# Performance work log

Measured on AMD Instinct MI355X. Metric: run time of the kernel, lower is better.

The kernel has to match this reference:

```python
import jax, jax.numpy as jnp
import numpy as np

N, C, L, E = 10000, 128, 9, 5  # nodes, channels, (lmax+1)^2, num_elements
INV_SQRT_C = 1.0 / np.sqrt(C).astype(np.float32)


def _sparse(key, shape, p=0.15):
    # mimic the sparsity of e3nn CG coupling (U) tensors
    k1, k2 = jax.random.split(key)
    mask = jax.random.bernoulli(k1, p, shape)
    vals = jax.random.normal(k2, shape, dtype=jnp.float32)
    return jnp.where(mask, vals, 0.0)


def setup_inputs() -> dict:
    key = jax.random.key(0)
    ks = jax.random.split(key, 16)
    node_feats = jax.random.normal(ks[0], (N, C, L), dtype=jnp.float32)
    node_attrs = jax.nn.one_hot(jax.random.randint(ks[1], (N,), 0, E), E, dtype=jnp.float32)
    sc = jax.random.normal(ks[2], (N, 512), dtype=jnp.float32)
    # CG coupling tensors U_nu per output irrep (constant buffers in the torch module)
    # l_out = 0 (d=1): path counts k3=10, k2=3, k1=1
    U3_0 = _sparse(ks[3], (1, L, L, L, 10))
    U2_0 = _sparse(ks[4], (1, L, L, 3))
    U1_0 = _sparse(ks[5], (1, L, 1))
    # l_out = 1 (d=3): path counts k3=12, k2=4, k1=1
    U3_1 = _sparse(ks[6], (3, L, L, L, 12))
    U2_1 = _sparse(ks[7], (3, L, L, 4))
    U1_1 = _sparse(ks[8], (3, L, 1))
    # element-dependent contraction weights: randn(E, k, C) / k  (MACE init)
    w3_0 = jax.random.normal(ks[9], (E, 10, C), dtype=jnp.float32) / 10.0
    w2_0 = jax.random.normal(ks[10], (E, 3, C), dtype=jnp.float32) / 3.0
    w1_0 = jax.random.normal(ks[11], (E, 1, C), dtype=jnp.float32) / 1.0
    w3_1 = jax.random.normal(ks[12], (E, 12, C), dtype=jnp.float32) / 12.0
    w2_1 = jax.random.normal(ks[13], (E, 4, C), dtype=jnp.float32) / 4.0
    w1_1 = jax.random.normal(ks[14], (E, 1, C), dtype=jnp.float32) / 1.0
    # o3.Linear internal weights (one [C,C] block per output irrep)
    kl0, kl1 = jax.random.split(ks[15])
    lin_w0 = jax.random.normal(kl0, (C, C), dtype=jnp.float32)
    lin_w1 = jax.random.normal(kl1, (C, C), dtype=jnp.float32)
    return dict(node_feats=node_feats, node_attrs=node_attrs, sc=sc,
                U3_0=U3_0, U2_0=U2_0, U1_0=U1_0, w3_0=w3_0, w2_0=w2_0, w1_0=w1_0,
                U3_1=U3_1, U2_1=U2_1, U1_1=U1_1, w3_1=w3_1, w2_1=w2_1, w1_1=w1_1,
                lin_w0=lin_w0, lin_w1=lin_w1)


def _contraction(x, y, U3, U2, U1, w3, w2, w1):
    # MACE recursive symmetric contraction, correlation=3.
    # x: [N,C,L] node feats, y: [N,E] one-hot, U_nu: [d, L^nu, k_nu], w_nu: [E,k_nu,C]
    out = jnp.einsum('duvwk,ekc,bcw,be->bcduv', U3, w3, x, y)      # [N,C,d,L,L]
    c2 = jnp.einsum('duvk,ekc,be->bcduv', U2, w2, y) + out
    out = jnp.einsum('bcduv,bcv->bcdu', c2, x)                      # [N,C,d,L]
    c1 = jnp.einsum('duk,ekc,be->bcdu', U1, w1, y) + out
    out = jnp.einsum('bcdu,bcu->bcd', c1, x)                        # [N,C,d]
    return out.reshape(out.shape[0], -1)                            # [N,C*d]


def reference(node_feats, node_attrs, sc,
              U3_0, U2_0, U1_0, w3_0, w2_0, w1_0,
              U3_1, U2_1, U1_1, w3_1, w2_1, w1_1,
              lin_w0, lin_w1):
    # SymmetricContraction: one Contraction per target irrep, concat over irreps
    out0 = _contraction(node_feats, node_attrs, U3_0, U2_0, U1_0, w3_0, w2_0, w1_0)  # [N,C]
    out1 = _contraction(node_feats, node_attrs, U3_1, U2_1, U1_1, w3_1, w2_1, w1_1)  # [N,3C]
    # o3.Linear(target_irreps, target_irreps): per-l channel mixing, 1/sqrt(fan_in)
    y0 = (out0 @ lin_w0) * INV_SQRT_C                                # [N,C]
    x1 = out1.reshape(-1, C, 3)
    y1 = jnp.einsum('bcd,ce->bed', x1, lin_w1) * INV_SQRT_C          # [N,C,3]
    out = jnp.concatenate([y0, y1.reshape(-1, 3 * C)], axis=-1)      # [N,512]
    return out + sc  # use_sc residual
```

## Files before the change

### kernel.cpp

```cpp
#include <hip/hip_runtime.h>


#define CCH 128
#define LDIM 9
#define NE 5
#define BLK 256
#define NCPT 4
#define TSTR 220
#define TGSTR 880
#define U3LDS 8748

__global__ __launch_bounds__(BLK) void count_offs_kernel(
    const float* __restrict__ attrs, int N,
    int* __restrict__ elem, int* __restrict__ gcnt,
    int* __restrict__ offs, int* __restrict__ cur) {
  int n = blockIdx.x * BLK + threadIdx.x;
  int e = 0;
  if (n < N) {
    const float* a = attrs + n * NE;
#pragma unroll
    for (int j = 1; j < NE; ++j)
      if (a[j] > 0.5f) e = j;
    elem[n] = e;
  }
  int lane = threadIdx.x & 63;
#pragma unroll
  for (int k = 0; k < NE; ++k) {
    unsigned long long m = __ballot(n < N && e == k);
    if (m) {
      int leader = __ffsll((long long)m) - 1;
      if (lane == leader) atomicAdd(&gcnt[k], __popcll(m));
    }
  }
  __threadfence();
  __syncthreads();
  if (threadIdx.x == 0) {
    int t = atomicAdd(&gcnt[NE], 1);
    if (t == (int)gridDim.x - 1) {
      int acc = 0;
      for (int k = 0; k < NE; ++k) {
        int ck = atomicAdd(&gcnt[k], 0);
        offs[k] = acc; cur[k] = acc; acc += ck;
      }
      offs[NE] = acc;
    }
  }
}

__global__ __launch_bounds__(BLK) void scatter_kernel(
    const int* __restrict__ elem, int N,
    int* __restrict__ cur, int* __restrict__ order) {
  int n = blockIdx.x * BLK + threadIdx.x;
  if (n >= N) return;
  int e = elem[n];
  int lane = threadIdx.x & 63;
#pragma unroll
  for (int k = 0; k < NE; ++k) {
    if (e == k) {
      unsigned long long m = __ballot(1);
      int cnt = __popcll(m);
      int leader = __ffsll((long long)m) - 1;
      int base = 0;
      if (lane == leader) base = atomicAdd(&cur[k], cnt);
      base = __shfl(base, leader);
      int rank = __popcll(m & ((1ull << lane) - 1ull));
      order[base + rank] = n;
    }
  }
}

__global__ __launch_bounds__(BLK) void table_kernel(
    const float* __restrict__ U3_0, const float* __restrict__ U2_0,
    const float* __restrict__ U1_0, const float* __restrict__ U3_1,
    const float* __restrict__ U2_1, const float* __restrict__ U1_1,
    const float* __restrict__ w3_0, const float* __restrict__ w2_0,
    const float* __restrict__ w1_0, const float* __restrict__ w3_1,
    const float* __restrict__ w2_1, const float* __restrict__ w1_1,
    float* __restrict__ table) {
  const int b = blockIdx.x;
  const int dd = blockIdx.y;
  const int e = b / CCH, c = b % CCH;
  float* Tg = table + (size_t)b * TGSTR + dd * TSTR;
  __shared__ float Us[U3LDS];
  __shared__ float U2s[324];
  __shared__ float R3[729];
  __shared__ float R2[81];
  __shared__ float R1l[9];
  __shared__ float w3l[12], w2l[4];
  const int tid = threadIdx.x;
  const int d = dd - 1;
  const int K3 = (dd == 0) ? 10 : 12;
  const int K2 = (dd == 0) ? 3 : 4;

  if (dd == 0) {
    for (int i = tid; i < 7290; i += BLK) Us[i] = U3_0[i];
    for (int i = tid; i < 243; i += BLK)  U2s[i] = U2_0[i];
    if (tid < 10) w3l[tid] = w3_0[(e * 10 + tid) * CCH + c];
    else if (tid < 13) w2l[tid - 10] = w2_0[(e * 3 + (tid - 10)) * CCH + c];
    if (tid < 9) R1l[tid] = U1_0[tid] * w1_0[e * CCH + c];
  } else {
    for (int i = tid; i < 8748; i += BLK) Us[i] = U3_1[d * 8748 + i];
    for (int i = tid; i < 324; i += BLK)  U2s[i] = U2_1[d * 324 + i];
    if (tid < 12) w3l[tid] = w3_1[(e * 12 + tid) * CCH + c];
    else if (tid < 16) w2l[tid - 12] = w2_1[(e * 4 + (tid - 12)) * CCH + c];
    if (tid < 9) R1l[tid] = U1_1[d * 9 + tid] * w1_1[e * CCH + c];
  }
  __syncthreads();
  for (int r = tid; r < 729; r += BLK) {
    float acc = 0.f;
    for (int k = 0; k < K3; ++k) acc += Us[r * K3 + k] * w3l[k];
    R3[r] = acc;
  }
  for (int q = tid; q < 81; q += BLK) {
    float acc = 0.f;
    for (int k = 0; k < K2; ++k) acc += U2s[q * K2 + k] * w2l[k];
    R2[q] = acc;
  }
  __syncthreads();
  for (int i = tid; i < TSTR; i += BLK) {
    float val = 0.f;
    if (i < 219) {
      int rem = i, u = 0;
      while (rem >= (10 - u) * (11 - u) / 2) {
        rem -= (10 - u) * (11 - u) / 2; ++u;
      }
      if (rem == 0) {
        val = R1l[u];
      } else {
        rem -= 1;
        int v = u;
        while (rem >= 10 - v) { rem -= 10 - v; ++v; }
        if (rem == 0) {
          val = (u == v) ? R2[u * 9 + v] : R2[u * 9 + v] + R2[v * 9 + u];
        } else {
          int w = v + (rem - 1);
          if (u == v && v == w)
            val = R3[(u * 9 + u) * 9 + u];
          else if (u == v)
            val = R3[(u * 9 + u) * 9 + w] + R3[(u * 9 + w) * 9 + u] +
                  R3[(w * 9 + u) * 9 + u];
          else if (v == w)
            val = R3[(u * 9 + v) * 9 + v] + R3[(v * 9 + u) * 9 + v] +
                  R3[(v * 9 + v) * 9 + u];
          else
            val = R3[(u * 9 + v) * 9 + w] + R3[(u * 9 + w) * 9 + v] +
                  R3[(v * 9 + u) * 9 + w] + R3[(v * 9 + w) * 9 + u] +
                  R3[(w * 9 + u) * 9 + v] + R3[(w * 9 + v) * 9 + u];
        }
      }
    }
    Tg[i] = val;
  }
}

__global__ __launch_bounds__(BLK, 6) void contract_kernel(
    const float* __restrict__ feats, const float* __restrict__ table,
    const int* __restrict__ order, const int* __restrict__ offs,
    float* __restrict__ tmp, int NPAD) {
  const int cg = blockIdx.x, e = blockIdx.z;
  const int c0 = cg * NCPT;
  const int start = offs[e], end = offs[e + 1];
  const int pbase = start + blockIdx.y * BLK;
  if (pbase >= end) return;
  const int p = pbase + threadIdx.x;
  const bool valid = (p < end);
  const int n = order[valid ? p : (end - 1)];

  float tf[NCPT * LDIM];
  {
    const float4* xp =
        (const float4*)(feats + ((size_t)n * CCH + c0) * LDIM);
#pragma unroll
    for (int q = 0; q < 9; ++q) *(float4*)&tf[4 * q] = xp[q];
  }

  const float* Te = table + (size_t)(e * CCH + c0) * TGSTR;

#pragma unroll 1
  for (int dd = 0; dd < 4; ++dd) {
    float accd[NCPT];
#pragma unroll
    for (int c = 0; c < NCPT; ++c) {
      const float* B = Te + (size_t)c * TGSTR + dd * TSTR;
      int idx = 0;
      float acc = 0.f;
#pragma unroll
      for (int u = 0; u < 9; ++u) {
        float inner = B[idx++];
#pragma unroll
        for (int v = u; v < 9; ++v) {
          float Hv = B[idx++];
#pragma unroll
          for (int w = v; w < 9; ++w)
            Hv = fmaf(B[idx++], tf[c * LDIM + w], Hv);
          inner = fmaf(Hv, tf[c * LDIM + v], inner);
        }
        acc = fmaf(inner, tf[c * LDIM + u], acc);
      }
      accd[c] = acc;
    }
    if (valid) {
      float* o = tmp + ((size_t)dd * CCH + c0) * NPAD + p;
#pragma unroll
      for (int c = 0; c < NCPT; ++c) o[(size_t)c * NPAD] = accd[c];
    }
  }
}

#define NB 8
__global__ __launch_bounds__(BLK, 6) void linear_kernel(
    const float* __restrict__ tmp, const float* __restrict__ W0,
    const float* __restrict__ W1, const float* __restrict__ sc,
    const int* __restrict__ order, float* __restrict__ out, int N, int NPAD) {
  const int p0 = blockIdx.x * NB;
  const int t = threadIdx.x;
  __shared__ __align__(16) float SU[4128];

#pragma unroll
  for (int k = 0; k < 4; ++k) {
    int f = t + k * BLK;
    int dd = f >> 8, r = f & 255;
    int ci = r >> 1, q = r & 1;
    float4 v = *(const float4*)(tmp + (size_t)(dd * CCH + ci) * NPAD + p0 + q * 4);
    *(float4*)(SU + dd * 1024 + ci * 8 + q * 4) = v;
  }
  __syncthreads();

  const int j = t & 7;
  const int o = t >> 3;
  float acc[4][4];
#pragma unroll
  for (int dd = 0; dd < 4; ++dd)
#pragma unroll
    for (int k = 0; k < 4; ++k) acc[dd][k] = 0.f;

  const float* W0p = W0 + o * 4;
  const float* W1p = W1 + o * 4;
#pragma unroll 4
  for (int ci = 0; ci < CCH; ++ci) {
    float a0 = SU[0 * 1024 + ci * 8 + j];
    float a1 = SU[1 * 1024 + ci * 8 + j];
    float a2 = SU[2 * 1024 + ci * 8 + j];
    float a3 = SU[3 * 1024 + ci * 8 + j];
    float4 wa = *(const float4*)(W0p + ci * CCH);
    float4 wc = *(const float4*)(W1p + ci * CCH);
    acc[0][0] = fmaf(a0, wa.x, acc[0][0]);
    acc[0][1] = fmaf(a0, wa.y, acc[0][1]);
    acc[0][2] = fmaf(a0, wa.z, acc[0][2]);
    acc[0][3] = fmaf(a0, wa.w, acc[0][3]);
    acc[1][0] = fmaf(a1, wc.x, acc[1][0]);
    acc[1][1] = fmaf(a1, wc.y, acc[1][1]);
    acc[1][2] = fmaf(a1, wc.z, acc[1][2]);
    acc[1][3] = fmaf(a1, wc.w, acc[1][3]);
    acc[2][0] = fmaf(a2, wc.x, acc[2][0]);
    acc[2][1] = fmaf(a2, wc.y, acc[2][1]);
    acc[2][2] = fmaf(a2, wc.z, acc[2][2]);
    acc[2][3] = fmaf(a2, wc.w, acc[2][3]);
    acc[3][0] = fmaf(a3, wc.x, acc[3][0]);
    acc[3][1] = fmaf(a3, wc.y, acc[3][1]);
    acc[3][2] = fmaf(a3, wc.z, acc[3][2]);
    acc[3][3] = fmaf(a3, wc.w, acc[3][3]);
  }
  __syncthreads();

  const float s = 0.08838834764831843f;
  float* Sj = SU + j * 516;
#pragma unroll
  for (int k = 0; k < 4; ++k) {
    int co = o * 4 + k;
    Sj[co]               = acc[0][k] * s;
    Sj[CCH + co * 3 + 0] = acc[1][k] * s;
    Sj[CCH + co * 3 + 1] = acc[2][k] * s;
    Sj[CCH + co * 3 + 2] = acc[3][k] * s;
  }
  __syncthreads();

  const int f = t & 127;
  const int jj = t >> 7;
#pragma unroll 1
  for (int jr = jj; jr < NB; jr += 2) {
    int p = p0 + jr;
    if (p < N) {
      int n = order[p];
      float4 sv = ((const float4*)(sc + (size_t)n * 512))[f];
      float4 ov = ((const float4*)(SU + jr * 516))[f];
      ov.x += sv.x; ov.y += sv.y; ov.z += sv.z; ov.w += sv.w;
      ((float4*)(out + (size_t)n * 512))[f] = ov;
    }
  }
}

extern "C" void kernel_launch(void* const* d_in, const int* in_sizes, int n_in,
                              void* d_out, int out_size, void* d_ws, size_t ws_size,
                              hipStream_t stream) {
  const float* feats = (const float*)d_in[0];
  const float* attrs = (const float*)d_in[1];
  const float* sc    = (const float*)d_in[2];
  const float* U3_0  = (const float*)d_in[3];
  const float* U2_0  = (const float*)d_in[4];
  const float* U1_0  = (const float*)d_in[5];
  const float* w3_0  = (const float*)d_in[6];
  const float* w2_0  = (const float*)d_in[7];
  const float* w1_0  = (const float*)d_in[8];
  const float* U3_1  = (const float*)d_in[9];
  const float* U2_1  = (const float*)d_in[10];
  const float* U1_1  = (const float*)d_in[11];
  const float* w3_1  = (const float*)d_in[12];
  const float* w2_1  = (const float*)d_in[13];
  const float* w1_1  = (const float*)d_in[14];
  const float* W0    = (const float*)d_in[15];
  const float* W1    = (const float*)d_in[16];

  const int N = in_sizes[0] / (CCH * LDIM);
  const int NPAD = ((N + 15) & ~15) + 16;

  float* table = (float*)d_ws;
  float* tmp   = table + (size_t)NE * CCH * TGSTR;
  int*   order = (int*)(tmp + (size_t)4 * CCH * NPAD);
  int*   elem  = order + N;
  int*   offs  = elem + N;
  int*   cur   = offs + 8;
  int*   gcnt  = cur + 8;
  float* out   = (float*)d_out;

  hipMemsetAsync(gcnt, 0, 8 * sizeof(int), stream);

  const int nblk = (N + BLK - 1) / BLK;
  count_offs_kernel<<<dim3(nblk), dim3(BLK), 0, stream>>>(
      attrs, N, elem, gcnt, offs, cur);
  scatter_kernel<<<dim3(nblk), dim3(BLK), 0, stream>>>(elem, N, cur, order);

  table_kernel<<<dim3(NE * CCH, 4), dim3(BLK), 0, stream>>>(
      U3_0, U2_0, U1_0, U3_1, U2_1, U1_1,
      w3_0, w2_0, w1_0, w3_1, w2_1, w1_1, table);

  const int chunks = (N + BLK - 1) / BLK;
  contract_kernel<<<dim3(CCH / NCPT, chunks, NE), dim3(BLK), 0, stream>>>(
      feats, table, order, offs, tmp, NPAD);

  linear_kernel<<<dim3((N + NB - 1) / NB), dim3(BLK), 0, stream>>>(
      tmp, W0, W1, sc, order, out, N, NPAD);
}
```

Baseline: 281.9 us.

## Use one channel per contract block, compact element grid, prefetch linear weights

The contraction kernel now handles one channel per thread instead of four and drops the per-element grid dimension. A flattened chunk index is mapped onto element segments, so far fewer blocks exit early, and register pressure falls enough to raise the occupancy hint. The linear kernel's inner loop is unrolled by two with register double-buffered prefetch of the weight rows, and its launch bound is lowered. Reading features per channel gives up the float4 loads, and each block must scan the offsets to find its segment.

```diff
diff --git a/kernel.cpp b/kernel.cpp
--- a/kernel.cpp
+++ b/kernel.cpp
@@ -5,7 +5,6 @@
 #define LDIM 9
 #define NE 5
 #define BLK 256
-#define NCPT 4
 #define TSTR 220
 #define TGSTR 880
 #define U3LDS 8748
@@ -153,62 +152,61 @@
   }
 }
 
-__global__ __launch_bounds__(BLK, 6) void contract_kernel(
+__global__ __launch_bounds__(BLK, 8) void contract_kernel(
     const float* __restrict__ feats, const float* __restrict__ table,
     const int* __restrict__ order, const int* __restrict__ offs,
     float* __restrict__ tmp, int NPAD) {
-  const int cg = blockIdx.x, e = blockIdx.z;
-  const int c0 = cg * NCPT;
-  const int start = offs[e], end = offs[e + 1];
-  const int pbase = start + blockIdx.y * BLK;
-  if (pbase >= end) return;
+  const int c = blockIdx.x;
+  int rem = blockIdx.y;
+  int e = -1, pbase = 0, segend = 0;
+#pragma unroll
+  for (int k = 0; k < NE; ++k) {
+    int st = offs[k], en = offs[k + 1];
+    int nc = (en - st + BLK - 1) >> 8;
+    if (e < 0) {
+      if (rem < nc) { e = k; pbase = st + rem * BLK; segend = en; }
+      else rem -= nc;
+    }
+  }
+  if (e < 0) return;
+
   const int p = pbase + threadIdx.x;
-  const bool valid = (p < end);
-  const int n = order[valid ? p : (end - 1)];
-
-  float tf[NCPT * LDIM];
+  const bool valid = (p < segend);
+  const int n = order[valid ? p : (segend - 1)];
+
+  float tf[LDIM];
   {
-    const float4* xp =
-        (const float4*)(feats + ((size_t)n * CCH + c0) * LDIM);
-#pragma unroll
-    for (int q = 0; q < 9; ++q) *(float4*)&tf[4 * q] = xp[q];
-  }
-
-  const float* Te = table + (size_t)(e * CCH + c0) * TGSTR;
+    const float* xp = feats + ((size_t)n * CCH + c) * LDIM;
+#pragma unroll
+    for (int q = 0; q < LDIM; ++q) tf[q] = xp[q];
+  }
+
+  const float* Tc = table + (size_t)(e * CCH + c) * TGSTR;
 
 #pragma unroll 1
   for (int dd = 0; dd < 4; ++dd) {
-    float accd[NCPT];
-#pragma unroll
-    for (int c = 0; c < NCPT; ++c) {
-      const float* B = Te + (size_t)c * TGSTR + dd * TSTR;
-      int idx = 0;
-      float acc = 0.f;
-#pragma unroll
-      for (int u = 0; u < 9; ++u) {
-        float inner = B[idx++];
-#pragma unroll
-        for (int v = u; v < 9; ++v) {
-          float Hv = B[idx++];
-#pragma unroll
-          for (int w = v; w < 9; ++w)
-            Hv = fmaf(B[idx++], tf[c * LDIM + w], Hv);
-          inner = fmaf(Hv, tf[c * LDIM + v], inner);
-        }
-        acc = fmaf(inner, tf[c * LDIM + u], acc);
+    const float* B = Tc + dd * TSTR;
+    int idx = 0;
+    float acc = 0.f;
+#pragma unroll
+    for (int u = 0; u < 9; ++u) {
+      float inner = B[idx++];
+#pragma unroll
+      for (int v = u; v < 9; ++v) {
+        float Hv = B[idx++];
+#pragma unroll
+        for (int w = v; w < 9; ++w)
+          Hv = fmaf(B[idx++], tf[w], Hv);
+        inner = fmaf(Hv, tf[v], inner);
       }
-      accd[c] = acc;
-    }
-    if (valid) {
-      float* o = tmp + ((size_t)dd * CCH + c0) * NPAD + p;
-#pragma unroll
-      for (int c = 0; c < NCPT; ++c) o[(size_t)c * NPAD] = accd[c];
-    }
+      acc = fmaf(inner, tf[u], acc);
+    }
+    if (valid) tmp[((size_t)dd * CCH + c) * NPAD + p] = acc;
   }
 }
 
 #define NB 8
-__global__ __launch_bounds__(BLK, 6) void linear_kernel(
+__global__ __launch_bounds__(BLK, 5) void linear_kernel(
     const float* __restrict__ tmp, const float* __restrict__ W0,
     const float* __restrict__ W1, const float* __restrict__ sc,
     const int* __restrict__ order, float* __restrict__ out, int N, int NPAD) {
@@ -236,30 +234,61 @@
 
   const float* W0p = W0 + o * 4;
   const float* W1p = W1 + o * 4;
-#pragma unroll 4
-  for (int ci = 0; ci < CCH; ++ci) {
+  float4 wa0 = *(const float4*)(W0p + 0 * CCH);
+  float4 wc0 = *(const float4*)(W1p + 0 * CCH);
+  float4 wa1 = *(const float4*)(W0p + 1 * CCH);
+  float4 wc1 = *(const float4*)(W1p + 1 * CCH);
+#pragma unroll 2
+  for (int ci = 0; ci < CCH; ci += 2) {
+    const int cn = (ci + 2) & 127;
+    float4 pa0 = *(const float4*)(W0p + cn * CCH);
+    float4 pc0 = *(const float4*)(W1p + cn * CCH);
+    float4 pa1 = *(const float4*)(W0p + (cn + 1) * CCH);
+    float4 pc1 = *(const float4*)(W1p + (cn + 1) * CCH);
+
     float a0 = SU[0 * 1024 + ci * 8 + j];
     float a1 = SU[1 * 1024 + ci * 8 + j];
     float a2 = SU[2 * 1024 + ci * 8 + j];
     float a3 = SU[3 * 1024 + ci * 8 + j];
-    float4 wa = *(const float4*)(W0p + ci * CCH);
-    float4 wc = *(const float4*)(W1p + ci * CCH);
-    acc[0][0] = fmaf(a0, wa.x, acc[0][0]);
-    acc[0][1] = fmaf(a0, wa.y, acc[0][1]);
-    acc[0][2] = fmaf(a0, wa.z, acc[0][2]);
-    acc[0][3] = fmaf(a0, wa.w, acc[0][3]);
-    acc[1][0] = fmaf(a1, wc.x, acc[1][0]);
-    acc[1][1] = fmaf(a1, wc.y, acc[1][1]);
-    acc[1][2] = fmaf(a1, wc.z, acc[1][2]);
-    acc[1][3] = fmaf(a1, wc.w, acc[1][3]);
-    acc[2][0] = fmaf(a2, wc.x, acc[2][0]);
-    acc[2][1] = fmaf(a2, wc.y, acc[2][1]);
-    acc[2][2] = fmaf(a2, wc.z, acc[2][2]);
-    acc[2][3] = fmaf(a2, wc.w, acc[2][3]);
-    acc[3][0] = fmaf(a3, wc.x, acc[3][0]);
-    acc[3][1] = fmaf(a3, wc.y, acc[3][1]);
-    acc[3][2] = fmaf(a3, wc.z, acc[3][2]);
-    acc[3][3] = fmaf(a3, wc.w, acc[3][3]);
+    acc[0][0] = fmaf(a0, wa0.x, acc[0][0]);
+    acc[0][1] = fmaf(a0, wa0.y, acc[0][1]);
+    acc[0][2] = fmaf(a0, wa0.z, acc[0][2]);
+    acc[0][3] = fmaf(a0, wa0.w, acc[0][3]);
+    acc[1][0] = fmaf(a1, wc0.x, acc[1][0]);
+    acc[1][1] = fmaf(a1, wc0.y, acc[1][1]);
+    acc[1][2] = fmaf(a1, wc0.z, acc[1][2]);
+    acc[1][3] = fmaf(a1, wc0.w, acc[1][3]);
+    acc[2][0] = fmaf(a2, wc0.x, acc[2][0]);
+    acc[2][1] = fmaf(a2, wc0.y, acc[2][1]);
+    acc[2][2] = fmaf(a2, wc0.z, acc[2][2]);
+    acc[2][3] = fmaf(a2, wc0.w, acc[2][3]);
+    acc[3][0] = fmaf(a3, wc0.x, acc[3][0]);
+    acc[3][1] = fmaf(a3, wc0.y, acc[3][1]);
+    acc[3][2] = fmaf(a3, wc0.z, acc[3][2]);
+    acc[3][3] = fmaf(a3, wc0.w, acc[3][3]);
+
+    float b0 = SU[0 * 1024 + (ci + 1) * 8 + j];
+    float b1 = SU[1 * 1024 + (ci + 1) * 8 + j];
+    float b2 = SU[2 * 1024 + (ci + 1) * 8 + j];
+    float b3 = SU[3 * 1024 + (ci + 1) * 8 + j];
+    acc[0][0] = fmaf(b0, wa1.x, acc[0][0]);
+    acc[0][1] = fmaf(b0, wa1.y, acc[0][1]);
+    acc[0][2] = fmaf(b0, wa1.z, acc[0][2]);
+    acc[0][3] = fmaf(b0, wa1.w, acc[0][3]);
+    acc[1][0] = fmaf(b1, wc1.x, acc[1][0]);
+    acc[1][1] = fmaf(b1, wc1.y, acc[1][1]);
+    acc[1][2] = fmaf(b1, wc1.z, acc[1][2]);
+    acc[1][3] = fmaf(b1, wc1.w, acc[1][3]);
+    acc[2][0] = fmaf(b2, wc1.x, acc[2][0]);
+    acc[2][1] = fmaf(b2, wc1.y, acc[2][1]);
+    acc[2][2] = fmaf(b2, wc1.z, acc[2][2]);
+    acc[2][3] = fmaf(b2, wc1.w, acc[2][3]);
+    acc[3][0] = fmaf(b3, wc1.x, acc[3][0]);
+    acc[3][1] = fmaf(b3, wc1.y, acc[3][1]);
+    acc[3][2] = fmaf(b3, wc1.z, acc[3][2]);
+    acc[3][3] = fmaf(b3, wc1.w, acc[3][3]);
+
+    wa0 = pa0; wc0 = pc0; wa1 = pa1; wc1 = pc1;
   }
   __syncthreads();
 
@@ -334,8 +363,8 @@
       U3_0, U2_0, U1_0, U3_1, U2_1, U1_1,
       w3_0, w2_0, w1_0, w3_1, w2_1, w1_1, table);
 
-  const int chunks = (N + BLK - 1) / BLK;
-  contract_kernel<<<dim3(CCH / NCPT, chunks, NE), dim3(BLK), 0, stream>>>(
+  const int chunksMax = (N + BLK - 1) / BLK + NE;
+  contract_kernel<<<dim3(CCH, chunksMax), dim3(BLK), 0, stream>>>(
       feats, table, order, offs, tmp, NPAD);
 
   linear_kernel<<<dim3((N + NB - 1) / NB), dim3(BLK), 0, stream>>>(
```

After: 266.4 us. 1.06x faster.
